# Kernel tuning notes

Measured on AMD Instinct MI355X. Metric: run time of the kernel, lower is better.

The kernel has to match this reference:

```python
import jax, jax.numpy as jnp
import numpy as np

NB_NODE = 100000
FT = 256
OUT_FT = 256
NB_REL = 4
BATCH = 8192
DEG = 16  # padded neighbors per (node, relation)


def setup_inputs() -> dict:
    key = jax.random.key(0)
    k1, k2, k3, k4 = jax.random.split(key, 4)
    features = jax.random.normal(k1, (NB_NODE, FT), dtype=jnp.float32)
    neighbor_idx = jax.random.randint(k2, (BATCH, NB_REL, DEG), 0, NB_NODE, dtype=jnp.int32)
    # per-relation GCN weight, scaled like xavier
    W = jax.random.normal(k3, (NB_REL, FT, OUT_FT), dtype=jnp.float32) * (1.0 / np.sqrt(FT))
    b = jnp.zeros((NB_REL, OUT_FT), dtype=jnp.float32)
    prelu_a = jnp.full((1,), 0.25, dtype=jnp.float32)  # nn.PReLU() default single param
    node_list = jax.random.randint(k4, (BATCH,), 0, NB_NODE, dtype=jnp.int32)
    return {"features": features, "neighbor_idx": neighbor_idx, "W": W, "b": b,
            "prelu_a": prelu_a, "node_list": node_list, "k": 0}


def _prelu(x, a):
    return jnp.where(x >= 0, x, a * x)


def reference(features, neighbor_idx, W, b, prelu_a, node_list, k):
    # Ragged per-relation neighbor gather + mean (vectorized form of the
    # python double loop): [B, R, D, F] -> mean over D -> [B, R, F]
    v_in = jnp.mean(features[neighbor_idx], axis=2)
    # Per-relation GCN linear + PReLU: [B, R, F] x [R, F, O] -> [B, R, O]
    h = jnp.einsum('brf,rfo->bro', v_in, W) + b[None, :, :]
    h = _prelu(h, prelu_a[0])
    # isAtt=False branch: mean over relations -> [B, O]
    return jnp.mean(h, axis=1)
```

## Files before the change

### kernel.cpp

```cpp
#include <hip/hip_runtime.h>
#include <hip/hip_bf16.h>

#define B_TOT 8192
#define FT    256
#define NREL  4
#define DEG   16

typedef __attribute__((ext_vector_type(8))) short bf16x8;
typedef __attribute__((ext_vector_type(4))) float f32x4;

static __device__ __forceinline__ unsigned short f2bf(float x) {
    union { float f; unsigned int u; } c; c.f = x;
    unsigned int u = c.u;
    u += 0x7fffu + ((u >> 16) & 1u);
    return (unsigned short)(u >> 16);
}
static __device__ __forceinline__ float bf2f(unsigned short h) {
    union { unsigned int u; float f; } c; c.u = ((unsigned int)h) << 16;
    return c.f;
}
static __device__ __forceinline__ int pack2(float lo, float hi) {
    return ((int)f2bf(hi) << 16) | (int)f2bf(lo);
}

__global__ __launch_bounds__(256) void cvt_feat_k(const float* __restrict__ f,
                                                  int* __restrict__ fb,
                                                  int n8) {
    int i = blockIdx.x * 256 + threadIdx.x;
    if (i < n8) {
        float4 a = ((const float4*)f)[i * 2];
        float4 b = ((const float4*)f)[i * 2 + 1];
        int4 o;
        o.x = pack2(a.x, a.y); o.y = pack2(a.z, a.w);
        o.z = pack2(b.x, b.y); o.w = pack2(b.z, b.w);
        ((int4*)fb)[i] = o;
    }
}

__global__ __launch_bounds__(256) void wtrans_k(const float* __restrict__ W,
                                                unsigned short* __restrict__ Wt) {
    __shared__ float t[64][65];
    int r = blockIdx.z, ft = blockIdx.y, ot = blockIdx.x;
    int c = threadIdx.x & 63, rw = threadIdx.x >> 6;
    const float* src = W + ((size_t)r * 256 + ft * 64) * 256 + ot * 64;
#pragma unroll
    for (int i = 0; i < 16; ++i) {
        int row = i * 4 + rw;
        t[row][c] = src[(size_t)row * 256 + c];
    }
    __syncthreads();
    unsigned short* dst = Wt + ((size_t)r * 256 + ot * 64) * 256 + ft * 64;
#pragma unroll
    for (int i = 0; i < 16; ++i) {
        int row = i * 4 + rw;
        dst[(size_t)row * 256 + c] = f2bf(t[c][row]);
    }
}

__global__ __launch_bounds__(256) void gather_mean_bf16_k(const unsigned short* __restrict__ fb,
                                                          const int* __restrict__ nidx,
                                                          unsigned short* __restrict__ v) {
    int wave = threadIdx.x >> 6;
    int lane = threadIdx.x & 63;
    int task = blockIdx.x * 4 + wave;
    int b = task >> 2, r = task & 3;
    const int* idx = nidx + ((size_t)b * NREL + r) * DEG;
    int4 i0 = *(const int4*)(idx);
    int4 i1 = *(const int4*)(idx + 4);
    int4 i2 = *(const int4*)(idx + 8);
    int4 i3 = *(const int4*)(idx + 12);
    float s0 = 0.f, s1 = 0.f, s2 = 0.f, s3 = 0.f;
#define ACC(nn) { const ushort4 x = ((const ushort4*)(fb + (size_t)(nn) * FT))[lane]; \
                  s0 += bf2f(x.x); s1 += bf2f(x.y); s2 += bf2f(x.z); s3 += bf2f(x.w); }
    ACC(i0.x) ACC(i0.y) ACC(i0.z) ACC(i0.w)
    ACC(i1.x) ACC(i1.y) ACC(i1.z) ACC(i1.w)
    ACC(i2.x) ACC(i2.y) ACC(i2.z) ACC(i2.w)
    ACC(i3.x) ACC(i3.y) ACC(i3.z) ACC(i3.w)
#undef ACC
    const float inv = 1.0f / 16.0f;
    ushort4 o;
    o.x = f2bf(s0 * inv); o.y = f2bf(s1 * inv);
    o.z = f2bf(s2 * inv); o.w = f2bf(s3 * inv);
    *(ushort4*)(v + ((size_t)r * B_TOT + b) * FT + 4 * lane) = o;
}

__global__ __launch_bounds__(256) void gather_mean_k(const float* __restrict__ feat,
                                                     const int* __restrict__ nidx,
                                                     unsigned short* __restrict__ v) {
    int wave = threadIdx.x >> 6;
    int lane = threadIdx.x & 63;
    int task = blockIdx.x * 4 + wave;
    int b = task >> 2, r = task & 3;
    const int* idx = nidx + ((size_t)b * NREL + r) * DEG;
    int4 i0 = *(const int4*)(idx);
    int4 i1 = *(const int4*)(idx + 4);
    int4 i2 = *(const int4*)(idx + 8);
    int4 i3 = *(const int4*)(idx + 12);
    float4 s = make_float4(0.f, 0.f, 0.f, 0.f);
#define ACC(nn) { const float4 x = ((const float4*)(feat + (size_t)(nn) * FT))[lane]; \
                  s.x += x.x; s.y += x.y; s.z += x.z; s.w += x.w; }
    ACC(i0.x) ACC(i0.y) ACC(i0.z) ACC(i0.w)
    ACC(i1.x) ACC(i1.y) ACC(i1.z) ACC(i1.w)
    ACC(i2.x) ACC(i2.y) ACC(i2.z) ACC(i2.w)
    ACC(i3.x) ACC(i3.y) ACC(i3.z) ACC(i3.w)
#undef ACC
    const float inv = 1.0f / 16.0f;
    ushort4 o;
    o.x = f2bf(s.x * inv); o.y = f2bf(s.y * inv);
    o.z = f2bf(s.z * inv); o.w = f2bf(s.w * inv);
    *(ushort4*)(v + ((size_t)r * B_TOT + b) * FT + 4 * lane) = o;
}

__global__ __launch_bounds__(256) void gemm_k(const unsigned short* __restrict__ v,
                                              const unsigned short* __restrict__ Wt,
                                              const float* __restrict__ bias,
                                              const float* __restrict__ prelu,
                                              float* __restrict__ out) {
    __shared__ unsigned short As[64][264];
    __shared__ unsigned short Bs[64][264];
    int tid  = threadIdx.x;
    int lane = tid & 63, w = tid >> 6;
    int wm = w >> 1, wn = w & 1;
    int mrow = lane & 15, quad = lane >> 4;
    int bid = blockIdx.x;
    int m0 = (bid & 127) * 64, n0 = (bid >> 7) * 64;
    float pa = prelu[0];

    f32x4 accO[2][2] = {};
    int ocol0 = n0 + wn * 32 + mrow;

    for (int r = 0; r < NREL; ++r) {
        const unsigned short* Ag = v  + ((size_t)r * B_TOT + m0) * FT;
        const unsigned short* Bg = Wt + ((size_t)r * 256  + n0) * FT;
#pragma unroll
        for (int i = 0; i < 8; ++i) {
            int u = tid + i * 256;
            int row = u >> 5, c8 = (u & 31) * 8;
            *(int4*)(&As[row][c8]) = *(const int4*)(Ag + row * FT + c8);
            *(int4*)(&Bs[row][c8]) = *(const int4*)(Bg + row * FT + c8);
        }
        __syncthreads();

        f32x4 acc[2][2] = {};
#pragma unroll
        for (int kk = 0; kk < 8; ++kk) {
            int k0 = kk * 32 + quad * 8;
            bf16x8 a0 = *(const bf16x8*)&As[wm * 32 + mrow][k0];
            bf16x8 a1 = *(const bf16x8*)&As[wm * 32 + 16 + mrow][k0];
            bf16x8 b0 = *(const bf16x8*)&Bs[wn * 32 + mrow][k0];
            bf16x8 b1 = *(const bf16x8*)&Bs[wn * 32 + 16 + mrow][k0];
            acc[0][0] = __builtin_amdgcn_mfma_f32_16x16x32_bf16(a0, b0, acc[0][0], 0, 0, 0);
            acc[1][0] = __builtin_amdgcn_mfma_f32_16x16x32_bf16(a1, b0, acc[1][0], 0, 0, 0);
            acc[0][1] = __builtin_amdgcn_mfma_f32_16x16x32_bf16(a0, b1, acc[0][1], 0, 0, 0);
            acc[1][1] = __builtin_amdgcn_mfma_f32_16x16x32_bf16(a1, b1, acc[1][1], 0, 0, 0);
        }
        __syncthreads();

        float b0v = bias[r * 256 + ocol0];
        float b1v = bias[r * 256 + ocol0 + 16];
#pragma unroll
        for (int mt = 0; mt < 2; ++mt)
#pragma unroll
            for (int i = 0; i < 4; ++i) {
                float h0 = acc[mt][0][i] + b0v; h0 = (h0 >= 0.f) ? h0 : pa * h0;
                float h1 = acc[mt][1][i] + b1v; h1 = (h1 >= 0.f) ? h1 : pa * h1;
                accO[mt][0][i] += h0;
                accO[mt][1][i] += h1;
            }
    }

#pragma unroll
    for (int mt = 0; mt < 2; ++mt)
#pragma unroll
        for (int i = 0; i < 4; ++i) {
            int row = m0 + wm * 32 + mt * 16 + quad * 4 + i;
            out[(size_t)row * 256 + ocol0]      = accO[mt][0][i] * 0.25f;
            out[(size_t)row * 256 + ocol0 + 16] = accO[mt][1][i] * 0.25f;
        }
}

extern "C" void kernel_launch(void* const* d_in, const int* in_sizes, int n_in,
                              void* d_out, int out_size, void* d_ws, size_t ws_size,
                              hipStream_t stream) {
    const float* feat  = (const float*)d_in[0];
    const int*   nidx  = (const int*)  d_in[1];
    const float* W     = (const float*)d_in[2];
    const float* bias  = (const float*)d_in[3];
    const float* prelu = (const float*)d_in[4];
    float* out = (float*)d_out;

    const size_t feat_elems = (size_t)in_sizes[0];
    const size_t fb_bytes = feat_elems * 2;
    const size_t v_bytes  = (size_t)NREL * B_TOT * FT * 2;
    const size_t wt_bytes = (size_t)NREL * 256 * FT * 2;

    if (ws_size >= fb_bytes + v_bytes + wt_bytes) {
        unsigned short* fb = (unsigned short*)d_ws;
        unsigned short* v  = fb + feat_elems;
        unsigned short* Wt = v + (size_t)NREL * B_TOT * FT;
        int n8 = (int)(feat_elems / 8);
        cvt_feat_k<<<(n8 + 255) / 256, 256, 0, stream>>>(feat, (int*)fb, n8);
        wtrans_k<<<dim3(4, 4, 4), 256, 0, stream>>>(W, Wt);
        gather_mean_bf16_k<<<B_TOT, 256, 0, stream>>>(fb, nidx, v);
        gemm_k<<<512, 256, 0, stream>>>(v, Wt, bias, prelu, out);
    } else {
        unsigned short* v  = (unsigned short*)d_ws;
        unsigned short* Wt = v + (size_t)NREL * B_TOT * FT;
        wtrans_k<<<dim3(4, 4, 4), 256, 0, stream>>>(W, Wt);
        gather_mean_k<<<B_TOT, 256, 0, stream>>>(feat, nidx, v);
        gemm_k<<<512, 256, 0, stream>>>(v, Wt, bias, prelu, out);
    }
}
```

Baseline: 214.7 us.

## Fuse neighbor gather-mean with per-relation GEMM and PReLU in one kernel

Replaces the separate bf16 gather-mean kernel and tiled GEMM with a single kernel. Each block gathers 16 batch rows across all 4 relations into shared memory, then runs MFMA against the transposed bf16 weights read directly from global memory (L2-resident) and applies bias, PReLU and the relation mean. This removes the global round-trip of the intermediate v tensor and one launch. The costs are only 512 blocks, each doing 16 serial gather iterations, and weight reads that are repeated per block with no shared-memory staging.

```diff
diff --git a/kernel.cpp b/kernel.cpp
--- a/kernel.cpp
+++ b/kernel.cpp
@@ -57,31 +57,76 @@
     }
 }
 
-__global__ __launch_bounds__(256) void gather_mean_bf16_k(const unsigned short* __restrict__ fb,
-                                                          const int* __restrict__ nidx,
-                                                          unsigned short* __restrict__ v) {
-    int wave = threadIdx.x >> 6;
-    int lane = threadIdx.x & 63;
-    int task = blockIdx.x * 4 + wave;
-    int b = task >> 2, r = task & 3;
-    const int* idx = nidx + ((size_t)b * NREL + r) * DEG;
-    int4 i0 = *(const int4*)(idx);
-    int4 i1 = *(const int4*)(idx + 4);
-    int4 i2 = *(const int4*)(idx + 8);
-    int4 i3 = *(const int4*)(idx + 12);
-    float s0 = 0.f, s1 = 0.f, s2 = 0.f, s3 = 0.f;
+__global__ __launch_bounds__(256) void fused_k(const unsigned short* __restrict__ fb,
+                                               const int* __restrict__ nidx,
+                                               const unsigned short* __restrict__ Wt,
+                                               const float* __restrict__ bias,
+                                               const float* __restrict__ prelu,
+                                               float* __restrict__ out) {
+    __shared__ unsigned short A[NREL][16][264];
+    int tid = threadIdx.x, lane = tid & 63, w = tid >> 6;
+    int blk = blockIdx.x;
+
+    for (int j = 0; j < 16; ++j) {
+        int b = blk * 16 + j;
+        const int* idx = nidx + ((size_t)b * NREL + w) * DEG;
+        int4 i0 = *(const int4*)(idx);
+        int4 i1 = *(const int4*)(idx + 4);
+        int4 i2 = *(const int4*)(idx + 8);
+        int4 i3 = *(const int4*)(idx + 12);
+        float s0 = 0.f, s1 = 0.f, s2 = 0.f, s3 = 0.f;
 #define ACC(nn) { const ushort4 x = ((const ushort4*)(fb + (size_t)(nn) * FT))[lane]; \
                   s0 += bf2f(x.x); s1 += bf2f(x.y); s2 += bf2f(x.z); s3 += bf2f(x.w); }
-    ACC(i0.x) ACC(i0.y) ACC(i0.z) ACC(i0.w)
-    ACC(i1.x) ACC(i1.y) ACC(i1.z) ACC(i1.w)
-    ACC(i2.x) ACC(i2.y) ACC(i2.z) ACC(i2.w)
-    ACC(i3.x) ACC(i3.y) ACC(i3.z) ACC(i3.w)
+        ACC(i0.x) ACC(i0.y) ACC(i0.z) ACC(i0.w)
+        ACC(i1.x) ACC(i1.y) ACC(i1.z) ACC(i1.w)
+        ACC(i2.x) ACC(i2.y) ACC(i2.z) ACC(i2.w)
+        ACC(i3.x) ACC(i3.y) ACC(i3.z) ACC(i3.w)
 #undef ACC
-    const float inv = 1.0f / 16.0f;
-    ushort4 o;
-    o.x = f2bf(s0 * inv); o.y = f2bf(s1 * inv);
-    o.z = f2bf(s2 * inv); o.w = f2bf(s3 * inv);
-    *(ushort4*)(v + ((size_t)r * B_TOT + b) * FT + 4 * lane) = o;
+        const float inv = 1.0f / 16.0f;
+        ushort4 o;
+        o.x = f2bf(s0 * inv); o.y = f2bf(s1 * inv);
+        o.z = f2bf(s2 * inv); o.w = f2bf(s3 * inv);
+        *(ushort4*)(&A[w][j][lane * 4]) = o;
+    }
+    __syncthreads();
+
+    int mrow = lane & 15, quad = lane >> 4;
+    float pa = prelu[0];
+    f32x4 accO[4] = {};
+#pragma unroll
+    for (int r = 0; r < NREL; ++r) {
+        f32x4 acc[4] = {};
+#pragma unroll
+        for (int kk = 0; kk < 8; ++kk) {
+            int k0 = kk * 32 + quad * 8;
+            bf16x8 a = *(const bf16x8*)&A[r][mrow][k0];
+#pragma unroll
+            for (int nt = 0; nt < 4; ++nt) {
+                int n = w * 64 + nt * 16 + mrow;
+                bf16x8 bf = *(const bf16x8*)(Wt + ((size_t)(r * 256 + n)) * 256 + k0);
+                acc[nt] = __builtin_amdgcn_mfma_f32_16x16x32_bf16(a, bf, acc[nt], 0, 0, 0);
+            }
+        }
+#pragma unroll
+        for (int nt = 0; nt < 4; ++nt) {
+            float bv = bias[r * 256 + w * 64 + nt * 16 + mrow];
+#pragma unroll
+            for (int i = 0; i < 4; ++i) {
+                float h = acc[nt][i] + bv;
+                h = (h >= 0.f) ? h : pa * h;
+                accO[nt][i] += h;
+            }
+        }
+    }
+#pragma unroll
+    for (int nt = 0; nt < 4; ++nt) {
+        int ocol = w * 64 + nt * 16 + mrow;
+#pragma unroll
+        for (int i = 0; i < 4; ++i) {
+            int row = blk * 16 + quad * 4 + i;
+            out[(size_t)row * 256 + ocol] = accO[nt][i] * 0.25f;
+        }
+    }
 }
 
 __global__ __launch_bounds__(256) void gather_mean_k(const float* __restrict__ feat,
@@ -191,21 +236,20 @@
 
     const size_t feat_elems = (size_t)in_sizes[0];
     const size_t fb_bytes = feat_elems * 2;
+    const size_t wt_bytes = (size_t)NREL * 256 * FT * 2;
     const size_t v_bytes  = (size_t)NREL * B_TOT * FT * 2;
-    const size_t wt_bytes = (size_t)NREL * 256 * FT * 2;
-
-    if (ws_size >= fb_bytes + v_bytes + wt_bytes) {
+
+    if (ws_size >= fb_bytes + wt_bytes) {
         unsigned short* fb = (unsigned short*)d_ws;
-        unsigned short* v  = fb + feat_elems;
-        unsigned short* Wt = v + (size_t)NREL * B_TOT * FT;
+        unsigned short* Wt = fb + feat_elems;
         int n8 = (int)(feat_elems / 8);
         cvt_feat_k<<<(n8 + 255) / 256, 256, 0, stream>>>(feat, (int*)fb, n8);
         wtrans_k<<<dim3(4, 4, 4), 256, 0, stream>>>(W, Wt);
-        gather_mean_bf16_k<<<B_TOT, 256, 0, stream>>>(fb, nidx, v);
-        gemm_k<<<512, 256, 0, stream>>>(v, Wt, bias, prelu, out);
+        fused_k<<<B_TOT / 16, 256, 0, stream>>>(fb, nidx, Wt, bias, prelu, out);
     } else {
         unsigned short* v  = (unsigned short*)d_ws;
         unsigned short* Wt = v + (size_t)NREL * B_TOT * FT;
+        (void)v_bytes;
         wtrans_k<<<dim3(4, 4, 4), 256, 0, stream>>>(W, Wt);
         gather_mean_k<<<B_TOT, 256, 0, stream>>>(feat, nidx, v);
         gemm_k<<<512, 256, 0, stream>>>(v, Wt, bias, prelu, out);
```

After: 252.6 us. +17.6%, slower.
